# Optimization experiments

Measured on AMD Instinct MI355X. Metric: run time of the kernel, lower is better.

The kernel has to match this reference:

```python
import jax, jax.numpy as jnp
import numpy as np

B, S, H, K, L, NH, FF = 4, 2048, 2048, 1024, 2, 16, 4096
EPS = 1e-5

def _alibi_slopes(n):
    # standard power-of-two ALiBi slopes
    start = 2.0 ** (-8.0 / n)
    return start ** jnp.arange(1, n + 1, dtype=jnp.float32)

def _layernorm(h, g, b):
    mu = jnp.mean(h, axis=-1, keepdims=True)
    var = jnp.mean(jnp.square(h - mu), axis=-1, keepdims=True)
    return (h - mu) * jax.lax.rsqrt(var + EPS) * g + b

def setup_inputs() -> dict:
    key = jax.random.key(0)
    ks = jax.random.split(key, 16)
    x = jax.random.normal(ks[0], (B, S, H), jnp.float32)
    prev = jax.random.normal(ks[1], (B, S, H), jnp.float32)
    # unique sorted token indices per batch row (jit-friendly boolean mask)
    idx = jnp.stack([jnp.sort(jax.random.permutation(jax.random.fold_in(ks[2], b), S)[:K])
                     for b in range(B)]).astype(jnp.int32)
    w = 0.02
    Wq = jax.random.normal(ks[3], (L, H, H), jnp.float32) * w
    Wk = jax.random.normal(ks[4], (L, H, H), jnp.float32) * w
    Wv = jax.random.normal(ks[5], (L, H, H), jnp.float32) * w
    Wo = jax.random.normal(ks[6], (L, H, H), jnp.float32) * w
    attn_gamma = jnp.ones((L, H), jnp.float32)
    attn_beta = jnp.zeros((L, H), jnp.float32)
    mlp_gamma = jnp.ones((L, H), jnp.float32)
    mlp_beta = jnp.zeros((L, H), jnp.float32)
    Wgate = jax.random.normal(ks[7], (L, H, FF), jnp.float32) * w
    Wup = jax.random.normal(ks[8], (L, H, FF), jnp.float32) * w
    Wdown = jax.random.normal(ks[9], (L, FF, H), jnp.float32) * w
    return {"x": x, "prev": prev, "idx": idx, "Wq": Wq, "Wk": Wk, "Wv": Wv,
            "Wo": Wo, "attn_gamma": attn_gamma, "attn_beta": attn_beta,
            "mlp_gamma": mlp_gamma, "mlp_beta": mlp_beta,
            "Wgate": Wgate, "Wup": Wup, "Wdown": Wdown}

def _forward(x, prev, idx, Wq, Wk, Wv, Wo, attn_gamma, attn_beta,
             mlp_gamma, mlp_beta, Wgate, Wup, Wdown):
    d = H // NH
    scale = 1.0 / jnp.sqrt(jnp.asarray(d, jnp.float32))
    # gather selected tokens: [B, K, H]
    cur = jnp.take_along_axis(x, idx[:, :, None], axis=1)
    mem = jnp.take_along_axis(prev, idx[:, :, None], axis=1)
    # non-causal ALiBi bias over selected-sequence positions: [NH, K, K]
    pos = jnp.arange(K)
    dist = jnp.abs(pos[:, None] - pos[None, :]).astype(jnp.float32)
    bias = -_alibi_slopes(NH)[:, None, None] * dist
    for l in range(L):
        q = (cur @ Wq[l]).reshape(B, K, NH, d)
        k = (mem @ Wk[l]).reshape(B, K, NH, d)
        v = (mem @ Wv[l]).reshape(B, K, NH, d)
        scores = jnp.einsum('bqhd,bkhd->bhqk', q, k) * scale + bias
        attn = jax.nn.softmax(scores, axis=-1)
        o = jnp.einsum('bhqk,bkhd->bqhd', attn, v).reshape(B, K, H) @ Wo[l]
        cur = cur + o
        normed = _layernorm(cur, attn_gamma[l], attn_beta[l])
        mlp = (jax.nn.silu(normed @ Wgate[l]) * (normed @ Wup[l])) @ Wdown[l]
        cur = cur + mlp
        cur = _layernorm(cur, mlp_gamma[l], mlp_beta[l])
    # scatter-add back: out[mask] += update_val
    out = x.at[jnp.arange(B)[:, None], idx].add(cur)
    return out

def reference(x, prev, idx, Wq, Wk, Wv, Wo, attn_gamma, attn_beta,
              mlp_gamma, mlp_beta, Wgate, Wup, Wdown):
    return _forward(x, prev, idx, Wq, Wk, Wv, Wo, attn_gamma, attn_beta,
                    mlp_gamma, mlp_beta, Wgate, Wup, Wdown)
```

## Files before the change

kernel.cpp:

```cpp
#include <hip/hip_runtime.h>
#include <hip/hip_bf16.h>

#define BB 4
#define SS 2048
#define HH 2048
#define KK 1024
#define LL 2
#define NHH 16
#define FFF 4096
#define DD 128

typedef __attribute__((ext_vector_type(8))) short s8v;
typedef __attribute__((ext_vector_type(4))) short s4v;
typedef __attribute__((ext_vector_type(4))) float f4v;

__device__ __forceinline__ short f2bf(float f) {
  unsigned u = __builtin_bit_cast(unsigned, f);
  u += 0x7fffu + ((u >> 16) & 1u);
  return (short)(u >> 16);
}
__device__ __forceinline__ float bf2f(short s) {
  unsigned u = ((unsigned)(unsigned short)s) << 16;
  return __builtin_bit_cast(float, u);
}
__device__ __forceinline__ f4v mfma16(s8v a, s8v b, f4v c) {
  asm("v_mfma_f32_16x16x32_bf16 %0, %1, %2, %0" : "+v"(c) : "v"(a), "v"(b));
  return c;
}
__device__ __forceinline__ void gload_lds16(const void* g, void* l) {
  __builtin_amdgcn_global_load_lds(
      (__attribute__((address_space(1))) void*)g,
      (__attribute__((address_space(3))) void*)l, 16, 0, 0);
}
template <int N>
__device__ __forceinline__ void barrier_cnt() {
  if constexpr (N == 3)
    asm volatile("s_waitcnt vmcnt(3) expcnt(0) lgkmcnt(0)" ::: "memory");
  else if constexpr (N == 4)
    asm volatile("s_waitcnt vmcnt(4) expcnt(0) lgkmcnt(0)" ::: "memory");
  else
    asm volatile("s_waitcnt vmcnt(0) expcnt(0) lgkmcnt(0)" ::: "memory");
  __builtin_amdgcn_s_barrier();
  asm volatile("" ::: "memory");
}

__global__ __launch_bounds__(256) void wconv(const float* __restrict__ W,
                                             short* __restrict__ Wt,
                                             int Kd, int N) {
  __shared__ short tile[64][65];
  int n0 = blockIdx.x * 64, k0 = blockIdx.y * 64;
  int t = threadIdx.x;
#pragma unroll
  for (int i = 0; i < 16; ++i) {
    int lin = i * 256 + t;
    int r = lin >> 6, c = lin & 63;
    tile[c][r] = f2bf(W[(size_t)(k0 + r) * N + n0 + c]);
  }
  __syncthreads();
#pragma unroll
  for (int i = 0; i < 16; ++i) {
    int lin = i * 256 + t;
    int r = lin >> 6, c = lin & 63;
    Wt[(size_t)(n0 + r) * Kd + k0 + c] = tile[r][c];
  }
}

__global__ __launch_bounds__(256) void gather_rows(
    const float* __restrict__ x, const float* __restrict__ prev,
    const int* __restrict__ idx, float* __restrict__ cur_f,
    short* __restrict__ cur_b, short* __restrict__ mem_b) {
  int r = blockIdx.x;
  int b = r >> 10, kk = r & (KK - 1);
  int src = idx[b * KK + kk];
  const float4* xs = (const float4*)(x + ((size_t)b * SS + src) * HH);
  const float4* ps = (const float4*)(prev + ((size_t)b * SS + src) * HH);
  float4* cf = (float4*)(cur_f + (size_t)r * HH);
  s4v* cb = (s4v*)(cur_b + (size_t)r * HH);
  s4v* mb = (s4v*)(mem_b + (size_t)r * HH);
  int t = threadIdx.x;
#pragma unroll
  for (int i = 0; i < 2; ++i) {
    int c = t + i * 256;
    float4 xv = xs[c], pv = ps[c];
    cf[c] = xv;
    s4v cv, mv;
    cv[0] = f2bf(xv.x); cv[1] = f2bf(xv.y); cv[2] = f2bf(xv.z); cv[3] = f2bf(xv.w);
    mv[0] = f2bf(pv.x); mv[1] = f2bf(pv.y); mv[2] = f2bf(pv.z); mv[3] = f2bf(pv.w);
    cb[c] = cv; mb[c] = mv;
  }
}

template <int EPI>
__global__ __launch_bounds__(512, 2) void g8p(
    const short* __restrict__ A, const short* __restrict__ Bt,
    float* __restrict__ Cf, short* __restrict__ Cb,
    int M, int N, int Kd) {
  __shared__ __align__(16) short smem[3 * 12288];
  const int t = threadIdx.x;
  const int w = t >> 6, l = t & 63;
  const int wr = w >> 2, wc = w & 3;
  const int l15 = l & 15, lh = l >> 4;
  const int koffs = (lh ^ ((l15 >> 1) & 3)) * 8;

  const int gx = gridDim.x, gy = gridDim.y;
  const int nwg = gx * gy;
  const int bid = blockIdx.y * gx + blockIdx.x;
  const int wg = (bid & 7) * (nwg >> 3) + (bid >> 3);
  const int by = wg & (gy - 1);
  const int bx = wg / gy;
  const int rowBase = by * 128, colBase = bx * 256;

  const int ar = t >> 2;
  const int ac = ((t & 3) ^ ((t >> 3) & 3)) * 8;
  const short* gA = A + (size_t)(rowBase + ar) * Kd + ac;
  const short* gB0 = Bt + (size_t)(colBase + ar) * Kd + ac;
  const short* gB1 = gB0 + (size_t)128 * Kd;
  const int lA = t * 8;
  const int lB = 4096 + t * 8;

  auto stage = [&](int bi, int kt) {
    const int k0 = kt * 32;
    short* base = smem + bi * 12288;
    gload_lds16(gA + k0, base + lA);
    gload_lds16(gB0 + k0, base + lB);
    gload_lds16(gB1 + k0, base + lB + 4096);
  };

  f4v acc[4][4];
#pragma unroll
  for (int i = 0; i < 4; ++i)
#pragma unroll
    for (int j = 0; j < 4; ++j) acc[i][j] = (f4v){0.f, 0.f, 0.f, 0.f};

  const int NT = Kd >> 5;
  stage(0, 0);
  stage(1, 1);
  barrier_cnt<3>();

  int cur = 0;
  for (int kt = 0; kt < NT; ++kt) {
    const short* sb = smem + cur * 12288;
    const bool more = (kt + 2 < NT);
    if (more) {
      int nb = cur + 2; if (nb >= 3) nb -= 3;
      stage(nb, kt + 2);
    }
    s8v af[4], bf[4];
#pragma unroll
    for (int mt = 0; mt < 4; ++mt)
      af[mt] = *(const s8v*)(sb + (wr * 64 + mt * 16 + l15) * 32 + koffs);
#pragma unroll
    for (int nt = 0; nt < 4; ++nt)
      bf[nt] = *(const s8v*)(sb + 4096 + (wc * 64 + nt * 16 + l15) * 32 + koffs);
#pragma unroll
    for (int mt = 0; mt < 4; ++mt)
#pragma unroll
      for (int nt = 0; nt < 4; ++nt)
        acc[mt][nt] = mfma16(af[mt], bf[nt], acc[mt][nt]);
    if (more) barrier_cnt<3>(); else barrier_cnt<0>();
    cur = (cur + 1 == 3) ? 0 : cur + 1;
  }

#pragma unroll
  for (int mt = 0; mt < 4; ++mt) {
#pragma unroll
    for (int nt = 0; nt < 4; ++nt) {
#pragma unroll
      for (int rr = 0; rr < 4; ++rr) {
        int row = rowBase + wr * 64 + mt * 16 + lh * 4 + rr;
        int col = colBase + wc * 64 + nt * 16 + l15;
        float v = acc[mt][nt][rr];
        if constexpr (EPI == 0) {
          Cb[(size_t)row * N + col] = f2bf(v);
        } else if constexpr (EPI == 1) {
          Cf[(size_t)row * N + col] += v;
        } else if constexpr (EPI == 2) {
          int b = row >> 10, ktok = row & (KK - 1);
          int h = col >> 7, dd = col & (DD - 1);
          Cb[(((size_t)(b * NHH + h)) * DD + dd) * KK + ktok] = f2bf(v);
        }
      }
    }
  }
}

template <int EPI>
__global__ __launch_bounds__(512, 2) void g256(
    const short* __restrict__ A, const short* __restrict__ Bt,
    short* __restrict__ Cb, short* __restrict__ Cb2, int M, int N, int Kd) {
  __shared__ __align__(16) short smem[3 * 16384];
  const int t = threadIdx.x;
  const int w = t >> 6, l = t & 63;
  const int wr = w >> 1, wc = w & 1;
  const int l15 = l & 15, lh = l >> 4;
  const int koffs = (lh ^ ((l15 >> 1) & 3)) * 8;

  const int gx = gridDim.x, gy = gridDim.y;
  const int nwg = gx * gy;
  const int bid = blockIdx.y * gx + blockIdx.x;
  const int wg = (bid & 7) * (nwg >> 3) + (bid >> 3);
  const int by = wg & (gy - 1);
  const int bx = wg / gy;
  const int rowBase = by * 256, colBase = bx * 256;

  const int ar = t >> 2;
  const int ac = ((t & 3) ^ ((t >> 3) & 3)) * 8;
  const short* gA = A + (size_t)(rowBase + ar) * Kd + ac;
  const short* gB = Bt + (size_t)(colBase + ar) * Kd + ac;
  const int lA = t * 8;
  const int lB = 8192 + t * 8;

  auto stage = [&](int bi, int kt) {
    const int k0 = kt * 32;
    short* base = smem + bi * 16384;
    gload_lds16(gA + k0, base + lA);
    gload_lds16(gA + k0 + (size_t)128 * Kd, base + lA + 4096);
    gload_lds16(gB + k0, base + lB);
    gload_lds16(gB + k0 + (size_t)128 * Kd, base + lB + 4096);
  };

  f4v acc[4][8];
#pragma unroll
  for (int i = 0; i < 4; ++i)
#pragma unroll
    for (int j = 0; j < 8; ++j) acc[i][j] = (f4v){0.f, 0.f, 0.f, 0.f};

  const int NT = Kd >> 5;
  stage(0, 0);
  stage(1, 1);
  barrier_cnt<4>();

  int cur = 0;
  for (int kt = 0; kt < NT; ++kt) {
    const short* sb = smem + cur * 16384;
    const bool more = (kt + 2 < NT);
    if (more) {
      int nb = cur + 2; if (nb >= 3) nb -= 3;
      stage(nb, kt + 2);
    }
    s8v af[4], bf[8];
#pragma unroll
    for (int mt = 0; mt < 4; ++mt)
      af[mt] = *(const s8v*)(sb + (wr * 64 + mt * 16 + l15) * 32 + koffs);
#pragma unroll
    for (int nt = 0; nt < 8; ++nt)
      bf[nt] = *(const s8v*)(sb + 8192 + (wc * 128 + nt * 16 + l15) * 32 + koffs);
#pragma unroll
    for (int mt = 0; mt < 4; ++mt)
#pragma unroll
      for (int nt = 0; nt < 8; ++nt)
        acc[mt][nt] = mfma16(af[mt], bf[nt], acc[mt][nt]);
    if (more) barrier_cnt<4>(); else barrier_cnt<0>();
    cur = (cur + 1 == 3) ? 0 : cur + 1;
  }

#pragma unroll
  for (int mt = 0; mt < 4; ++mt) {
#pragma unroll
    for (int nt = 0; nt < 8; ++nt) {
#pragma unroll
      for (int rr = 0; rr < 4; ++rr) {
        int row = rowBase + wr * 64 + mt * 16 + lh * 4 + rr;
        int col = colBase + wc * 128 + nt * 16 + l15;
        float v = acc[mt][nt][rr];
        if constexpr (EPI == 5) {
          if (col < HH) {
            Cb[(size_t)row * HH + col] = f2bf(v);
          } else {
            int vcol = col - HH;
            int b = row >> 10, ktok = row & (KK - 1);
            int h = vcol >> 7, dd = vcol & (DD - 1);
            Cb2[(((size_t)(b * NHH + h)) * DD + dd) * KK + ktok] = f2bf(v);
          }
        } else if constexpr (EPI == 6) {
          if (col < FFF) {
            float sv = v / (1.f + __expf(-v));
            Cb[(size_t)row * FFF + col] = f2bf(sv);
          } else {
            Cb2[(size_t)row * FFF + (col - FFF)] = f2bf(v);
          }
        }
      }
    }
  }
}

__global__ __launch_bounds__(256) void mul_bf16(short* __restrict__ hid,
                                                const short* __restrict__ sg,
                                                size_t n8) {
  size_t i = (size_t)blockIdx.x * 256 + threadIdx.x;
  size_t stride = (size_t)gridDim.x * 256;
  for (; i < n8; i += stride) {
    s8v a = ((const s8v*)hid)[i];
    s8v b = ((const s8v*)sg)[i];
    s8v o;
#pragma unroll
    for (int j = 0; j < 8; ++j) o[j] = f2bf(bf2f(a[j]) * bf2f(b[j]));
    ((s8v*)hid)[i] = o;
  }
}

__device__ __forceinline__ float exp2fast(float x) {
  float r;
  asm("v_exp_f32 %0, %1\n\ts_nop 0" : "=v"(r) : "v"(x));
  return r;
}
__global__ __launch_bounds__(256, 2) void attn_fwd(
    const short* __restrict__ qb, const short* __restrict__ kb,
    const short* __restrict__ vT, short* __restrict__ ob) {
  __shared__ __align__(16) short Kl[64 * 136];
  __shared__ __align__(16) short Vl[128 * 72];
  __shared__ __align__(16) short Pl[64 * 72];
  int b = blockIdx.z, h = blockIdx.y, qt = blockIdx.x;
  int t = threadIdx.x, w = t >> 6, l = t & 63, l15 = l & 15, lh = l >> 4;
  const float LOG2E = 1.4426950408889634f;
  float slope2 = exp2f(-0.5f * (float)(h + 1)) * LOG2E;
  const float c1 = 0.08838834764831845f * LOG2E;

  s8v qf[4];
  int qrowA = qt * 64 + w * 16 + l15;
  const short* qptr = qb + ((size_t)(b * KK + qrowA)) * HH + h * DD + lh * 8;
#pragma unroll
  for (int ks = 0; ks < 4; ++ks) qf[ks] = *(const s8v*)(qptr + ks * 32);

  f4v oacc[8];
#pragma unroll
  for (int i = 0; i < 8; ++i) oacc[i] = (f4v){0.f, 0.f, 0.f, 0.f};
  float m[4], sden[4];
#pragma unroll
  for (int r = 0; r < 4; ++r) { m[r] = -1e30f; sden[r] = 0.f; }
  int qpos_base = qt * 64 + w * 16 + lh * 4;

  for (int kt = 0; kt < KK / 64; ++kt) {
    {
      int rr = t >> 4, cc = (t & 15) * 8;
#pragma unroll
      for (int it = 0; it < 4; ++it) {
        int krow = it * 16 + rr;
        s8v g = *(const s8v*)(kb + ((size_t)(b * KK + kt * 64 + krow)) * HH + h * DD + cc);
        *(s8v*)&Kl[krow * 136 + cc] = g;
      }
      int dr = t >> 3, c2 = (t & 7) * 8;
#pragma unroll
      for (int it = 0; it < 4; ++it) {
        int drow = it * 32 + dr;
        s8v g = *(const s8v*)(vT + (((size_t)(b * NHH + h)) * DD + drow) * KK + kt * 64 + c2);
        *(s8v*)&Vl[drow * 72 + c2] = g;
      }
    }
    __syncthreads();

    f4v sacc[4];
#pragma unroll
    for (int ct = 0; ct < 4; ++ct) sacc[ct] = (f4v){0.f, 0.f, 0.f, 0.f};
#pragma unroll
    for (int ct = 0; ct < 4; ++ct)
#pragma unroll
      for (int ks = 0; ks < 4; ++ks) {
        s8v kf = *(const s8v*)&Kl[(ct * 16 + l15) * 136 + ks * 32 + lh * 8];
        sacc[ct] = mfma16(qf[ks], kf, sacc[ct]);
      }

#pragma unroll
    for (int r = 0; r < 4; ++r) {
      int qpos = qpos_base + r;
      float mx = -1e30f;
#pragma unroll
      for (int ct = 0; ct < 4; ++ct) {
        int kpos = kt * 64 + ct * 16 + l15;
        float sv = sacc[ct][r] * c1 - slope2 * fabsf((float)(qpos - kpos));
        sacc[ct][r] = sv;
        mx = fmaxf(mx, sv);
      }
      mx = fmaxf(mx, __shfl_xor(mx, 1));
      mx = fmaxf(mx, __shfl_xor(mx, 2));
      mx = fmaxf(mx, __shfl_xor(mx, 4));
      mx = fmaxf(mx, __shfl_xor(mx, 8));
      float mn = fmaxf(m[r], mx);
      float corr = exp2fast(m[r] - mn);
      m[r] = mn;
      float ps = 0.f;
#pragma unroll
      for (int ct = 0; ct < 4; ++ct) {
        float p = exp2fast(sacc[ct][r] - mn);
        sacc[ct][r] = p;
        ps += p;
      }
      ps += __shfl_xor(ps, 1); ps += __shfl_xor(ps, 2);
      ps += __shfl_xor(ps, 4); ps += __shfl_xor(ps, 8);
      sden[r] = sden[r] * corr + ps;
#pragma unroll
      for (int dt = 0; dt < 8; ++dt) oacc[dt][r] *= corr;
#pragma unroll
      for (int ct = 0; ct < 4; ++ct)
        Pl[(w * 16 + lh * 4 + r) * 72 + ct * 16 + l15] = f2bf(sacc[ct][r]);
    }

#pragma unroll
    for (int ks2 = 0; ks2 < 2; ++ks2) {
      s8v pa = *(const s8v*)&Pl[(w * 16 + l15) * 72 + ks2 * 32 + lh * 8];
#pragma unroll
      for (int dt = 0; dt < 8; ++dt) {
        s8v vf = *(const s8v*)&Vl[(dt * 16 + l15) * 72 + ks2 * 32 + lh * 8];
        oacc[dt] = mfma16(pa, vf, oacc[dt]);
      }
    }
    __syncthreads();
  }

#pragma unroll
  for (int dt = 0; dt < 8; ++dt)
#pragma unroll
    for (int r = 0; r < 4; ++r) {
      int qpos = qpos_base + r;
      int dd = dt * 16 + l15;
      ob[((size_t)(b * KK + qpos)) * HH + h * DD + dd] = f2bf(oacc[dt][r] / sden[r]);
    }
}

__global__ __launch_bounds__(256) void ln_rows(const float* in,
    const float* __restrict__ gma, const float* __restrict__ bta,
    short* __restrict__ outb, float* outf) {
  __shared__ float red[2][4];
  int r = blockIdx.x, t = threadIdx.x;
  const float4* x4 = (const float4*)(in + (size_t)r * HH);
  float4 va = x4[t], vb = x4[t + 256];
  float sum = va.x + va.y + va.z + va.w + vb.x + vb.y + vb.z + vb.w;
  float sq = va.x * va.x + va.y * va.y + va.z * va.z + va.w * va.w +
             vb.x * vb.x + vb.y * vb.y + vb.z * vb.z + vb.w * vb.w;
#pragma unroll
  for (int off = 32; off; off >>= 1) {
    sum += __shfl_down(sum, off);
    sq += __shfl_down(sq, off);
  }
  int w = t >> 6;
  if ((t & 63) == 0) { red[0][w] = sum; red[1][w] = sq; }
  __syncthreads();
  sum = red[0][0] + red[0][1] + red[0][2] + red[0][3];
  sq = red[1][0] + red[1][1] + red[1][2] + red[1][3];
  float mu = sum * (1.f / HH);
  float rs = rsqrtf(sq * (1.f / HH) - mu * mu + 1e-5f);
  const float4* g4 = (const float4*)gma;
  const float4* b4 = (const float4*)bta;
  s4v* ob = (s4v*)(outb + (size_t)r * HH);
  float4* of = (float4*)(outf ? outf + (size_t)r * HH : nullptr);
#pragma unroll
  for (int i = 0; i < 2; ++i) {
    int c = t + i * 256;
    float4 v = (i == 0) ? va : vb;
    float4 g = g4[c], bb = b4[c];
    float4 nv;
    nv.x = (v.x - mu) * rs * g.x + bb.x;
    nv.y = (v.y - mu) * rs * g.y + bb.y;
    nv.z = (v.z - mu) * rs * g.z + bb.z;
    nv.w = (v.w - mu) * rs * g.w + bb.w;
    s4v o;
    o[0] = f2bf(nv.x); o[1] = f2bf(nv.y); o[2] = f2bf(nv.z); o[3] = f2bf(nv.w);
    ob[c] = o;
    if (outf) of[c] = nv;
  }
}

__global__ __launch_bounds__(256) void copy_out(const float* __restrict__ x,
                                                float* __restrict__ out, size_t n4) {
  size_t i = (size_t)blockIdx.x * 256 + threadIdx.x;
  size_t stride = (size_t)gridDim.x * 256;
  const float4* xi = (const float4*)x;
  float4* oi = (float4*)out;
  for (; i < n4; i += stride) oi[i] = xi[i];
}

__global__ __launch_bounds__(256) void scatter_add(const int* __restrict__ idx,
                                                   const float* __restrict__ cur,
                                                   float* out) {
  int r = blockIdx.x;
  int b = r >> 10, kk = r & (KK - 1);
  int dst = idx[b * KK + kk];
  float4* o = (float4*)(out + ((size_t)b * SS + dst) * HH);
  const float4* c = (const float4*)(cur + (size_t)r * HH);
  int t = threadIdx.x;
#pragma unroll
  for (int i = 0; i < 2; ++i) {
    int j = t + i * 256;
    float4 ov = o[j], cv = c[j];
    ov.x += cv.x; ov.y += cv.y; ov.z += cv.z; ov.w += cv.w;
    o[j] = ov;
  }
}

extern "C" void kernel_launch(void* const* d_in, const int* in_sizes, int n_in,
                              void* d_out, int out_size, void* d_ws, size_t ws_size,
                              hipStream_t stream) {
  (void)in_sizes; (void)n_in; (void)out_size; (void)ws_size;
  const float* x = (const float*)d_in[0];
  const float* prv = (const float*)d_in[1];
  const int* idx = (const int*)d_in[2];
  const float* Wq = (const float*)d_in[3];
  const float* Wk = (const float*)d_in[4];
  const float* Wv = (const float*)d_in[5];
  const float* Wo = (const float*)d_in[6];
  const float* ag = (const float*)d_in[7];
  const float* ab = (const float*)d_in[8];
  const float* mg = (const float*)d_in[9];
  const float* mbt = (const float*)d_in[10];
  const float* Wg = (const float*)d_in[11];
  const float* Wu = (const float*)d_in[12];
  const float* Wd = (const float*)d_in[13];
  float* out = (float*)d_out;

  char* ws = (char*)d_ws;
  size_t off = 0;
  auto alloc = [&](size_t bytes) -> void* {
    void* p = ws + off;
    off += (bytes + 255) & ~(size_t)255;
    return p;
  };
  const size_t WHH = (size_t)HH * HH, WHF = (size_t)HH * FFF;
  short* WqT = (short*)alloc(LL * WHH * 2);
  short* WkvT = (short*)alloc(LL * 2 * WHH * 2);
  short* WoT = (short*)alloc(LL * WHH * 2);
  short* WguT = (short*)alloc(LL * 2 * WHF * 2);
  short* WdT = (short*)alloc(LL * WHF * 2);
  const size_t RH = (size_t)BB * KK * HH;
  float* cur_f = (float*)alloc(RH * 4);
  short* q_b = (short*)alloc(RH * 2);
  short* k_b = (short*)alloc(RH * 2);
  short* vT_b = (short*)alloc(RH * 2);
  short* o_b = (short*)alloc(RH * 2);
  short* cur_b = (short*)alloc(RH * 2);
  short* mem_b = (short*)alloc(RH * 2);
  short* nrm_b = (short*)alloc(RH * 2);
  short* sg_b = q_b;
  short* hid_b = vT_b;

  dim3 blk(256), blk512(512);
  for (int l = 0; l < LL; ++l) {
    wconv<<<dim3(HH / 64, HH / 64), blk, 0, stream>>>(Wq + l * WHH, WqT + l * WHH, HH, HH);
    wconv<<<dim3(HH / 64, HH / 64), blk, 0, stream>>>(Wk + l * WHH, WkvT + l * 2 * WHH, HH, HH);
    wconv<<<dim3(HH / 64, HH / 64), blk, 0, stream>>>(Wv + l * WHH, WkvT + l * 2 * WHH + WHH, HH, HH);
    wconv<<<dim3(HH / 64, HH / 64), blk, 0, stream>>>(Wo + l * WHH, WoT + l * WHH, HH, HH);
    wconv<<<dim3(FFF / 64, HH / 64), blk, 0, stream>>>(Wg + l * WHF, WguT + l * 2 * WHF, HH, FFF);
    wconv<<<dim3(FFF / 64, HH / 64), blk, 0, stream>>>(Wu + l * WHF, WguT + l * 2 * WHF + WHF, HH, FFF);
    wconv<<<dim3(HH / 64, FFF / 64), blk, 0, stream>>>(Wd + l * WHF, WdT + l * WHF, FFF, HH);
  }
  gather_rows<<<dim3(BB * KK), blk, 0, stream>>>(x, prv, idx, cur_f, cur_b, mem_b);

  const int M = BB * KK;
  for (int l = 0; l < LL; ++l) {
    const short* wq = WqT + l * WHH;
    const short* wkv = WkvT + l * 2 * WHH;
    const short* wo = WoT + l * WHH;
    const short* wgu = WguT + l * 2 * WHF;
    const short* wd = WdT + l * WHF;
    g8p<0><<<dim3(HH / 256, M / 128), blk512, 0, stream>>>(cur_b, wq, nullptr, q_b, M, HH, HH);
    g256<5><<<dim3(2 * HH / 256, M / 256), blk512, 0, stream>>>(mem_b, wkv, k_b, vT_b, M, 2 * HH, HH);
    attn_fwd<<<dim3(KK / 64, NHH, BB), blk, 0, stream>>>(q_b, k_b, vT_b, o_b);
    g8p<1><<<dim3(HH / 256, M / 128), blk512, 0, stream>>>(o_b, wo, cur_f, nullptr, M, HH, HH);
    ln_rows<<<dim3(M), blk, 0, stream>>>(cur_f, ag + l * HH, ab + l * HH, nrm_b, nullptr);
    g256<6><<<dim3(2 * FFF / 256, M / 256), blk512, 0, stream>>>(nrm_b, wgu, sg_b, hid_b, M, 2 * FFF, HH);
    mul_bf16<<<dim3(2048), blk, 0, stream>>>(hid_b, sg_b, RH * 2 / 8);
    g8p<1><<<dim3(HH / 256, M / 128), blk512, 0, stream>>>(hid_b, wd, cur_f, nullptr, M, HH, FFF);
    ln_rows<<<dim3(M), blk, 0, stream>>>(cur_f, mg + l * HH, mbt + l * HH, cur_b, cur_f);
  }
  copy_out<<<dim3(2048), blk, 0, stream>>>(x, out, (size_t)BB * SS * HH / 4);
  scatter_add<<<dim3(M), blk, 0, stream>>>(idx, cur_f, out);
}
```

Measured before the change: 1.319 ms.

## Interleave gate/up weight rows and fuse SiLU-multiply into gate-up GEMM epilogue

Gate and up weight rows are interleaved in 16-row groups during weight conversion, so each wave's accumulator tiles hold matching gate and up columns side by side. The GEMM epilogue then computes silu(gate)*up directly and writes one half-width hidden tensor. This removes the separate elementwise multiply kernel and the round trip of the two intermediate bf16 tensors. It also skips the bf16 rounding of the gate and up values before the multiply, which slightly changes numerics.

```diff
diff --git a/kernel.cpp b/kernel.cpp
--- a/kernel.cpp
+++ b/kernel.cpp
@@ -46,7 +46,7 @@
 
 __global__ __launch_bounds__(256) void wconv(const float* __restrict__ W,
                                              short* __restrict__ Wt,
-                                             int Kd, int N) {
+                                             int Kd, int N, int rowmap) {
   __shared__ short tile[64][65];
   int n0 = blockIdx.x * 64, k0 = blockIdx.y * 64;
   int t = threadIdx.x;
@@ -61,7 +61,9 @@
   for (int i = 0; i < 16; ++i) {
     int lin = i * 256 + t;
     int r = lin >> 6, c = lin & 63;
-    Wt[(size_t)(n0 + r) * Kd + k0 + c] = tile[r][c];
+    int n = n0 + r;
+    int nf = (rowmap == 0) ? n : (((n & ~15) << 1) + (n & 15) + (rowmap == 2 ? 16 : 0));
+    Wt[(size_t)nf * Kd + k0 + c] = tile[r][c];
   }
 }
 
@@ -256,14 +258,14 @@
 
 #pragma unroll
   for (int mt = 0; mt < 4; ++mt) {
-#pragma unroll
-    for (int nt = 0; nt < 8; ++nt) {
-#pragma unroll
-      for (int rr = 0; rr < 4; ++rr) {
-        int row = rowBase + wr * 64 + mt * 16 + lh * 4 + rr;
-        int col = colBase + wc * 128 + nt * 16 + l15;
-        float v = acc[mt][nt][rr];
-        if constexpr (EPI == 5) {
+    if constexpr (EPI == 5) {
+#pragma unroll
+      for (int nt = 0; nt < 8; ++nt) {
+#pragma unroll
+        for (int rr = 0; rr < 4; ++rr) {
+          int row = rowBase + wr * 64 + mt * 16 + lh * 4 + rr;
+          int col = colBase + wc * 128 + nt * 16 + l15;
+          float v = acc[mt][nt][rr];
           if (col < HH) {
             Cb[(size_t)row * HH + col] = f2bf(v);
           } else {
@@ -272,31 +274,23 @@
             int h = vcol >> 7, dd = vcol & (DD - 1);
             Cb2[(((size_t)(b * NHH + h)) * DD + dd) * KK + ktok] = f2bf(v);
           }
-        } else if constexpr (EPI == 6) {
-          if (col < FFF) {
-            float sv = v / (1.f + __expf(-v));
-            Cb[(size_t)row * FFF + col] = f2bf(sv);
-          } else {
-            Cb2[(size_t)row * FFF + (col - FFF)] = f2bf(v);
-          }
         }
       }
-    }
-  }
-}
-
-__global__ __launch_bounds__(256) void mul_bf16(short* __restrict__ hid,
-                                                const short* __restrict__ sg,
-                                                size_t n8) {
-  size_t i = (size_t)blockIdx.x * 256 + threadIdx.x;
-  size_t stride = (size_t)gridDim.x * 256;
-  for (; i < n8; i += stride) {
-    s8v a = ((const s8v*)hid)[i];
-    s8v b = ((const s8v*)sg)[i];
-    s8v o;
-#pragma unroll
-    for (int j = 0; j < 8; ++j) o[j] = f2bf(bf2f(a[j]) * bf2f(b[j]));
-    ((s8v*)hid)[i] = o;
+    } else {
+#pragma unroll
+      for (int nt = 0; nt < 8; nt += 2) {
+#pragma unroll
+        for (int rr = 0; rr < 4; ++rr) {
+          int row = rowBase + wr * 64 + mt * 16 + lh * 4 + rr;
+          int c = colBase + wc * 128 + nt * 16 + l15;
+          int j = ((c >> 5) << 4) | (c & 15);
+          float g = acc[mt][nt][rr];
+          float u = acc[mt][nt + 1][rr];
+          float h = (g / (1.f + __expf(-g))) * u;
+          Cb[(size_t)row * FFF + j] = f2bf(h);
+        }
+      }
+    }
   }
 }
 
@@ -530,18 +524,17 @@
   short* cur_b = (short*)alloc(RH * 2);
   short* mem_b = (short*)alloc(RH * 2);
   short* nrm_b = (short*)alloc(RH * 2);
-  short* sg_b = q_b;
   short* hid_b = vT_b;
 
   dim3 blk(256), blk512(512);
   for (int l = 0; l < LL; ++l) {
-    wconv<<<dim3(HH / 64, HH / 64), blk, 0, stream>>>(Wq + l * WHH, WqT + l * WHH, HH, HH);
-    wconv<<<dim3(HH / 64, HH / 64), blk, 0, stream>>>(Wk + l * WHH, WkvT + l * 2 * WHH, HH, HH);
-    wconv<<<dim3(HH / 64, HH / 64), blk, 0, stream>>>(Wv + l * WHH, WkvT + l * 2 * WHH + WHH, HH, HH);
-    wconv<<<dim3(HH / 64, HH / 64), blk, 0, stream>>>(Wo + l * WHH, WoT + l * WHH, HH, HH);
-    wconv<<<dim3(FFF / 64, HH / 64), blk, 0, stream>>>(Wg + l * WHF, WguT + l * 2 * WHF, HH, FFF);
-    wconv<<<dim3(FFF / 64, HH / 64), blk, 0, stream>>>(Wu + l * WHF, WguT + l * 2 * WHF + WHF, HH, FFF);
-    wconv<<<dim3(HH / 64, FFF / 64), blk, 0, stream>>>(Wd + l * WHF, WdT + l * WHF, FFF, HH);
+    wconv<<<dim3(HH / 64, HH / 64), blk, 0, stream>>>(Wq + l * WHH, WqT + l * WHH, HH, HH, 0);
+    wconv<<<dim3(HH / 64, HH / 64), blk, 0, stream>>>(Wk + l * WHH, WkvT + l * 2 * WHH, HH, HH, 0);
+    wconv<<<dim3(HH / 64, HH / 64), blk, 0, stream>>>(Wv + l * WHH, WkvT + l * 2 * WHH + WHH, HH, HH, 0);
+    wconv<<<dim3(HH / 64, HH / 64), blk, 0, stream>>>(Wo + l * WHH, WoT + l * WHH, HH, HH, 0);
+    wconv<<<dim3(FFF / 64, HH / 64), blk, 0, stream>>>(Wg + l * WHF, WguT + l * 2 * WHF, HH, FFF, 1);
+    wconv<<<dim3(FFF / 64, HH / 64), blk, 0, stream>>>(Wu + l * WHF, WguT + l * 2 * WHF, HH, FFF, 2);
+    wconv<<<dim3(HH / 64, FFF / 64), blk, 0, stream>>>(Wd + l * WHF, WdT + l * WHF, FFF, HH, 0);
   }
   gather_rows<<<dim3(BB * KK), blk, 0, stream>>>(x, prv, idx, cur_f, cur_b, mem_b);
 
@@ -557,8 +550,7 @@
     attn_fwd<<<dim3(KK / 64, NHH, BB), blk, 0, stream>>>(q_b, k_b, vT_b, o_b);
     g8p<1><<<dim3(HH / 256, M / 128), blk512, 0, stream>>>(o_b, wo, cur_f, nullptr, M, HH, HH);
     ln_rows<<<dim3(M), blk, 0, stream>>>(cur_f, ag + l * HH, ab + l * HH, nrm_b, nullptr);
-    g256<6><<<dim3(2 * FFF / 256, M / 256), blk512, 0, stream>>>(nrm_b, wgu, sg_b, hid_b, M, 2 * FFF, HH);
-    mul_bf16<<<dim3(2048), blk, 0, stream>>>(hid_b, sg_b, RH * 2 / 8);
+    g256<7><<<dim3(2 * FFF / 256, M / 256), blk512, 0, stream>>>(nrm_b, wgu, hid_b, nullptr, M, 2 * FFF, HH);
     g8p<1><<<dim3(HH / 256, M / 128), blk512, 0, stream>>>(hid_b, wd, cur_f, nullptr, M, HH, FFF);
     ln_rows<<<dim3(M), blk, 0, stream>>>(cur_f, mg + l * HH, mbt + l * HH, cur_b, cur_f);
   }
```

Result: faster. 1.265 ms (-4.1%).
